# Optimization experiments

Measured on AMD Instinct MI355X. Metric: run time of the kernel, lower is better.

## Reference

```python
import jax, jax.numpy as jnp
import numpy as np

B, D, F, S, R = 2048, 1024, 1024, 64, 16


def _lora_dense(x, ids, kernel, bias, la, lb):
    # base: frozen dense path (stop_gradient mirrors the original module)
    base = x @ jax.lax.stop_gradient(kernel)
    if bias is not None:
        base = base + jax.lax.stop_gradient(bias)
    a = la[ids]            # (B, D, R) per-example adapter gather
    b = lb[ids]            # (B, R, F)
    low = jnp.einsum('bd,bdr->br', x, a)
    delta = jnp.einsum('br,brf->bf', low, b)
    return base + delta


def setup_inputs() -> dict:
    key = jax.random.key(0)
    ks = jax.random.split(key, 32)
    i = iter(range(32))
    d = {}
    d['carry'] = jax.random.normal(ks[next(i)], (B, F), jnp.float32)
    d['inputs'] = jax.random.normal(ks[next(i)], (B, D), jnp.float32)
    d['adapter_ids'] = jax.random.randint(ks[next(i)], (B,), 0, S)
    kscale = 1.0 / np.sqrt(D)
    for g in ['ir', 'iu', 'ic']:
        d[f'w_{g}'] = jax.random.normal(ks[next(i)], (D, F), jnp.float32) * kscale
        d[f'bias_{g}'] = jax.random.normal(ks[next(i)], (F,), jnp.float32) * 0.01
        d[f'la_{g}'] = jax.random.normal(ks[next(i)], (S, D, R), jnp.float32) * 0.02
        d[f'lb_{g}'] = jax.random.normal(ks[next(i)], (S, R, F), jnp.float32) * 0.01
    for g in ['rr', 'ru', 'rc']:
        d[f'w_{g}'] = jax.random.normal(ks[next(i)], (F, F), jnp.float32) * kscale
        d[f'la_{g}'] = jax.random.normal(ks[next(i)], (S, F, R), jnp.float32) * 0.02
        d[f'lb_{g}'] = jax.random.normal(ks[next(i)], (S, R, F), jnp.float32) * 0.01
    return d


def reference(carry, inputs, adapter_ids,
              w_ir, bias_ir, la_ir, lb_ir,
              w_iu, bias_iu, la_iu, lb_iu,
              w_ic, bias_ic, la_ic, lb_ic,
              w_rr, la_rr, lb_rr,
              w_ru, la_ru, lb_ru,
              w_rc, la_rc, lb_rc):
    ids = adapter_ids
    reset = jax.nn.sigmoid(
        _lora_dense(inputs, ids, w_ir, bias_ir, la_ir, lb_ir)
        + _lora_dense(carry, ids, w_rr, None, la_rr, lb_rr))
    update = jax.nn.sigmoid(
        _lora_dense(inputs, ids, w_iu, bias_iu, la_iu, lb_iu)
        + _lora_dense(carry, ids, w_ru, None, la_ru, lb_ru))
    candidate = jnp.tanh(
        _lora_dense(inputs, ids, w_ic, bias_ic, la_ic, lb_ic)
        + reset * _lora_dense(carry, ids, w_rc, None, la_rc, lb_rc))
    new_carry = (1.0 - update) * candidate + update * carry
    return new_carry
```

## Files before the change

kernel.cpp:

```cpp
#include <hip/hip_runtime.h>
#include <stdint.h>

#define B_  2048
#define D_  1024
#define F_  1024
#define S_  64
#define R_  16

typedef __attribute__((ext_vector_type(8))) short  s16x8;
typedef __attribute__((ext_vector_type(4))) unsigned short u16x4;
typedef __attribute__((ext_vector_type(8))) unsigned short u16x8;
typedef __attribute__((ext_vector_type(4))) float  f32x4;

__device__ __forceinline__ unsigned short f2b(float f){
  unsigned u = __float_as_uint(f);
  u = u + 0x7fffu + ((u >> 16) & 1u);
  return (unsigned short)(u >> 16);
}
__device__ __forceinline__ float b2f(unsigned short s){
  return __uint_as_float(((unsigned)s) << 16);
}

__device__ __forceinline__ void gload16(const void* g, void* l){
  __builtin_amdgcn_global_load_lds((const __attribute__((address_space(1))) unsigned int*)g,
                                   (__attribute__((address_space(3))) unsigned int*)l, 16, 0, 0);
}

#define W0OFF 0
#define W1OFF 2097152
#define W2OFF 4194304
#define W3OFF 5242880

__global__ __launch_bounds__(256) void prep_kernel(
    const float* __restrict__ x, const float* __restrict__ carry,
    unsigned short* __restrict__ XC,
    const float* __restrict__ w_ir, const float* __restrict__ w_rr,
    const float* __restrict__ w_iu, const float* __restrict__ w_ru,
    const float* __restrict__ w_ic, const float* __restrict__ w_rc,
    unsigned short* __restrict__ Wt_all,
    const int* __restrict__ ids, int* __restrict__ starts, int* __restrict__ order){
  int bx = blockIdx.x;
  int t = threadIdx.x;
  if (bx < 2048){
    int i = bx * 256 + t;
    int b = i >> 8;
    int j = (i & 255) * 4;
    float4 xv = *(const float4*)&x[(size_t)b*D_ + j];
    float4 cv = *(const float4*)&carry[(size_t)b*F_ + j];
    u16x4 xs, cs;
    xs[0]=f2b(xv.x); xs[1]=f2b(xv.y); xs[2]=f2b(xv.z); xs[3]=f2b(xv.w);
    cs[0]=f2b(cv.x); cs[1]=f2b(cv.y); cs[2]=f2b(cv.z); cs[3]=f2b(cv.w);
    *(u16x4*)&XC[(size_t)b*2048 + j]        = xs;
    *(u16x4*)&XC[(size_t)b*2048 + 1024 + j] = cs;
    return;
  }
  if (bx < 3584){
    int wb = bx - 2048;
    int g = wb >> 8, xb = wb & 255;
    const float* W; unsigned short* O; int st, ko;
    switch(g){
      case 0:  W=w_ir; O=Wt_all+W0OFF; st=2048; ko=0;    break;
      case 1:  W=w_rr; O=Wt_all+W0OFF; st=2048; ko=1024; break;
      case 2:  W=w_iu; O=Wt_all+W1OFF; st=2048; ko=0;    break;
      case 3:  W=w_ru; O=Wt_all+W1OFF; st=2048; ko=1024; break;
      case 4:  W=w_ic; O=Wt_all+W2OFF; st=1024; ko=0;    break;
      default: W=w_rc; O=Wt_all+W3OFF; st=1024; ko=0;    break;
    }
    __shared__ unsigned short T[64][72];
    int n0 = (xb & 15) * 64;
    int k0 = (xb >> 4) * 64;
    int c4 = (t & 15) * 4;
    int kk = t >> 4;
    #pragma unroll
    for (int i = 0; i < 4; i++){
      int k = kk + i*16;
      float4 v = *(const float4*)&W[(size_t)(k0+k)*F_ + n0 + c4];
      T[c4+0][k] = f2b(v.x); T[c4+1][k] = f2b(v.y); T[c4+2][k] = f2b(v.z); T[c4+3][k] = f2b(v.w);
    }
    __syncthreads();
    int n = t >> 2, ch = (t & 3) * 16;
    u16x8 a = *(const u16x8*)&T[n][ch];
    u16x8 b = *(const u16x8*)&T[n][ch+8];
    *(u16x8*)&O[(size_t)(n0+n)*st + ko + k0 + ch]     = a;
    *(u16x8*)&O[(size_t)(n0+n)*st + ko + k0 + ch + 8] = b;
    return;
  }
  __shared__ int cnt[S_]; __shared__ int off[S_+1]; __shared__ int cur[S_];
  if (t < S_) cnt[t] = 0;
  __syncthreads();
  for (int b = t; b < B_; b += 256) atomicAdd(&cnt[ids[b]], 1);
  __syncthreads();
  if (t == 0){ off[0] = 0; for (int s2 = 0; s2 < S_; s2++) off[s2+1] = off[s2] + cnt[s2]; }
  __syncthreads();
  if (t < S_) cur[t] = off[t];
  __syncthreads();
  for (int b = t; b < B_; b += 256){ int p = atomicAdd(&cur[ids[b]], 1); order[p] = b; }
  if (t < S_+1) starts[t] = off[t];
}

__global__ __launch_bounds__(256, 4) void gemm_low_kernel(
    const unsigned short* __restrict__ XC,
    const unsigned short* __restrict__ Wt_all,
    unsigned short* __restrict__ Yall,
    const float* __restrict__ la_ir, const float* __restrict__ la_iu,
    const float* __restrict__ la_ic, const float* __restrict__ la_rr,
    const float* __restrict__ la_ru, const float* __restrict__ la_rc,
    const int* __restrict__ starts, const int* __restrict__ order,
    float* __restrict__ low){
  __shared__ __align__(16) unsigned short smem[16512];
  int t = threadIdx.x;
  int bx = blockIdx.x;

  if (bx >= 512){
    int lb = bx - 512;
    int s = lb & 63, g = lb >> 6;
    const float* la;
    switch(g){ case 0: la=la_ir; break; case 1: la=la_iu; break; case 2: la=la_ic; break;
               case 3: la=la_rr; break; case 4: la=la_ru; break; default: la=la_rc; break; }
    int kofs = (g < 3) ? 0 : 1024;
    la += (size_t)s * D_ * R_;
    unsigned short* LA = smem;
    for (int i4 = t; i4 < D_*R_/4; i4 += 256){
      float4 v = *(const float4*)&la[i4*4];
      int d = i4 >> 2, r0 = (i4 & 3) * 4;
      LA[(r0+0)*1032 + d] = f2b(v.x);
      LA[(r0+1)*1032 + d] = f2b(v.y);
      LA[(r0+2)*1032 + d] = f2b(v.z);
      LA[(r0+3)*1032 + d] = f2b(v.w);
    }
    __syncthreads();
    int start = starts[s], cnt = starts[s+1] - start;
    if (cnt == 0) return;
    int lane = t & 63, wave = t >> 6;
    int l15 = lane & 15, kq = (lane >> 4) * 8;
    int ntiles = (cnt + 15) >> 4;
    for (int mt = wave*2; mt < ntiles; mt += 8){
      bool two = (mt + 1 < ntiles);
      int m0 = mt*16 + l15;       if (m0 >= cnt) m0 = cnt - 1;
      int m1 = (mt+1)*16 + l15;   if (m1 >= cnt) m1 = cnt - 1;
      int e0 = order[start + m0];
      int e1 = two ? order[start + m1] : e0;
      const unsigned short* A0 = XC + (size_t)e0*2048 + kofs + kq;
      const unsigned short* A1 = XC + (size_t)e1*2048 + kofs + kq;
      const unsigned short* Bp = &LA[l15*1032 + kq];
      f32x4 acc0 = {}, acc1 = {};
      #pragma unroll 4
      for (int kt = 0; kt < 1024; kt += 32){
        s16x8 a0 = *(const s16x8*)(A0 + kt);
        s16x8 a1 = *(const s16x8*)(A1 + kt);
        s16x8 b  = *(const s16x8*)(Bp + kt);
        acc0 = __builtin_amdgcn_mfma_f32_16x16x32_bf16(a0, b, acc0, 0, 0, 0);
        acc1 = __builtin_amdgcn_mfma_f32_16x16x32_bf16(a1, b, acc1, 0, 0, 0);
      }
      int rowb = (lane >> 4) * 4;
      #pragma unroll
      for (int i = 0; i < 4; i++){
        int m = mt*16 + rowb + i;
        if (m < cnt){
          int e = order[start + m];
          low[((size_t)g*B_ + e)*R_ + l15] = acc0[i];
        }
      }
      if (two){
        #pragma unroll
        for (int i = 0; i < 4; i++){
          int m = (mt+1)*16 + rowb + i;
          if (m < cnt){
            int e = order[start + m];
            low[((size_t)g*B_ + e)*R_ + l15] = acc1[i];
          }
        }
      }
    }
    return;
  }

  int u = bx >> 7;
  int tile = bx & 127;
  int K = (u < 2) ? 2048 : 1024;
  int kofs = (u == 3) ? 1024 : 0;
  const size_t uoffs[4] = {W0OFF, W1OFF, W2OFF, W3OFF};
  const unsigned short* Wt = Wt_all + uoffs[u];
  unsigned short* Y = Yall + (size_t)u * ((size_t)B_ * F_);

  unsigned short (*As)[4096] = (unsigned short(*)[4096])smem;
  unsigned short (*Bs)[4096] = (unsigned short(*)[4096])(smem + 8192);

  int lane = t & 63, wave = t >> 6;
  int mt = tile >> 3, nt = tile & 7;
  int row0 = mt * 128, col0 = nt * 128;
  int wrow = (wave >> 1) * 64, wcol = (wave & 1) * 64;

  int arow = t >> 2;
  int achk = ((t & 3) ^ ((t >> 3) & 3)) * 8;

  const unsigned short* Ab  = XC + (size_t)(row0 + arow) * 2048 + kofs + achk;
  const unsigned short* Ab2 = Ab + (size_t)64 * 2048;
  const unsigned short* Bb  = Wt + (size_t)(col0 + arow) * K + achk;
  const unsigned short* Bb2 = Bb + (size_t)64 * K;

  int l15 = lane & 15;
  int kof = (((lane >> 4) ^ ((l15 >> 1) & 3)) * 8);
  f32x4 acc[4][4] = {};

  gload16(Ab,  &As[0][t*8]);  gload16(Ab2, &As[0][2048 + t*8]);
  gload16(Bb,  &Bs[0][t*8]);  gload16(Bb2, &Bs[0][2048 + t*8]);
  __syncthreads();

  int cur = 0;
  for (int kt = 32; kt < K; kt += 32){
    int nxt = cur ^ 1;
    gload16(Ab  + kt, &As[nxt][t*8]);  gload16(Ab2 + kt, &As[nxt][2048 + t*8]);
    gload16(Bb  + kt, &Bs[nxt][t*8]);  gload16(Bb2 + kt, &Bs[nxt][2048 + t*8]);
    s16x8 af[4], bfr[4];
    #pragma unroll
    for (int m = 0; m < 4; m++)
      af[m] = *(const s16x8*)&As[cur][(wrow + m*16 + l15)*32 + kof];
    #pragma unroll
    for (int n = 0; n < 4; n++)
      bfr[n] = *(const s16x8*)&Bs[cur][(wcol + n*16 + l15)*32 + kof];
    __builtin_amdgcn_s_setprio(1);
    #pragma unroll
    for (int m = 0; m < 4; m++){
      #pragma unroll
      for (int n = 0; n < 4; n++){
        acc[m][n] = __builtin_amdgcn_mfma_f32_16x16x32_bf16(af[m], bfr[n], acc[m][n], 0, 0, 0);
      }
    }
    __builtin_amdgcn_s_setprio(0);
    __syncthreads();
    cur = nxt;
  }
  {
    s16x8 af[4], bfr[4];
    #pragma unroll
    for (int m = 0; m < 4; m++)
      af[m] = *(const s16x8*)&As[cur][(wrow + m*16 + l15)*32 + kof];
    #pragma unroll
    for (int n = 0; n < 4; n++)
      bfr[n] = *(const s16x8*)&Bs[cur][(wcol + n*16 + l15)*32 + kof];
    #pragma unroll
    for (int m = 0; m < 4; m++){
      #pragma unroll
      for (int n = 0; n < 4; n++){
        acc[m][n] = __builtin_amdgcn_mfma_f32_16x16x32_bf16(af[m], bfr[n], acc[m][n], 0, 0, 0);
      }
    }
  }

  int orow = row0 + wrow + (lane >> 4) * 4;
  int ocol = col0 + wcol + l15;
  #pragma unroll
  for (int m = 0; m < 4; m++){
    #pragma unroll
    for (int n = 0; n < 4; n++){
      #pragma unroll
      for (int i = 0; i < 4; i++){
        Y[(size_t)(orow + m*16 + i) * F_ + ocol + n*16] = f2b(acc[m][n][i]);
      }
    }
  }
}

__global__ __launch_bounds__(256) void delta_final_kernel(
    const float* __restrict__ carry,
    const float* __restrict__ bias_ir, const float* __restrict__ bias_iu,
    const float* __restrict__ bias_ic,
    const float* __restrict__ lb_ir, const float* __restrict__ lb_rr,
    const float* __restrict__ lb_iu, const float* __restrict__ lb_ru,
    const float* __restrict__ lb_ic, const float* __restrict__ lb_rc,
    const int* __restrict__ starts, const int* __restrict__ order,
    const float* __restrict__ low, const unsigned short* __restrict__ Yall,
    float* __restrict__ out){
  int s = blockIdx.x;
  int c0 = blockIdx.y * 128;
  __shared__ unsigned short Bsm[3 * 128 * 40];
  int t = threadIdx.x;
  const float* lbp[6] = {lb_ir, lb_rr, lb_iu, lb_ru, lb_ic, lb_rc};
  #pragma unroll
  for (int j = 0; j < 6; j++){
    const float* lb = lbp[j] + (size_t)s * R_ * F_;
    unsigned short* Bj = &Bsm[(j >> 1)*5120 + (j & 1)*16];
    #pragma unroll
    for (int it = 0; it < 2; it++){
      int idx = t + it*256;
      int r = idx >> 5, c4 = (idx & 31) * 4;
      float4 v = *(const float4*)&lb[(size_t)r*F_ + c0 + c4];
      Bj[(c4+0)*40 + r] = f2b(v.x);
      Bj[(c4+1)*40 + r] = f2b(v.y);
      Bj[(c4+2)*40 + r] = f2b(v.z);
      Bj[(c4+3)*40 + r] = f2b(v.w);
    }
  }
  __syncthreads();
  int start = starts[s], cnt = starts[s+1] - start;
  if (cnt == 0) return;
  int lane = t & 63, wave = t >> 6;
  int l15 = lane & 15, kq = (lane >> 4) * 8;
  int ntiles = (cnt + 15) >> 4;
  const unsigned short* Y0 = Yall + 0*(size_t)B_*F_;
  const unsigned short* Y1 = Yall + 1*(size_t)B_*F_;
  const unsigned short* Y2 = Yall + 2*(size_t)B_*F_;
  const unsigned short* Y3 = Yall + 3*(size_t)B_*F_;
  int k8 = kq & 15; bool hi = (kq >= 16);
  for (int pt = wave; pt < ntiles*2; pt += 4){
    int mt = pt >> 1, cf0 = (pt & 1) * 4;
    int m = mt*16 + l15; if (m >= cnt) m = cnt - 1;
    int e = order[start + m];
    s16x8 a_r, a_u, a_c1 = {}, a_c2 = {};
    {
      const float* p = &low[((size_t)(hi ? 3 : 0)*B_ + e)*R_ + k8];
      float4 v0 = *(const float4*)p, v1 = *(const float4*)(p+4);
      a_r[0]=f2b(v0.x); a_r[1]=f2b(v0.y); a_r[2]=f2b(v0.z); a_r[3]=f2b(v0.w);
      a_r[4]=f2b(v1.x); a_r[5]=f2b(v1.y); a_r[6]=f2b(v1.z); a_r[7]=f2b(v1.w);
    }
    {
      const float* p = &low[((size_t)(hi ? 4 : 1)*B_ + e)*R_ + k8];
      float4 v0 = *(const float4*)p, v1 = *(const float4*)(p+4);
      a_u[0]=f2b(v0.x); a_u[1]=f2b(v0.y); a_u[2]=f2b(v0.z); a_u[3]=f2b(v0.w);
      a_u[4]=f2b(v1.x); a_u[5]=f2b(v1.y); a_u[6]=f2b(v1.z); a_u[7]=f2b(v1.w);
    }
    if (!hi){
      const float* p = &low[((size_t)2*B_ + e)*R_ + k8];
      float4 v0 = *(const float4*)p, v1 = *(const float4*)(p+4);
      a_c1[0]=f2b(v0.x); a_c1[1]=f2b(v0.y); a_c1[2]=f2b(v0.z); a_c1[3]=f2b(v0.w);
      a_c1[4]=f2b(v1.x); a_c1[5]=f2b(v1.y); a_c1[6]=f2b(v1.z); a_c1[7]=f2b(v1.w);
    } else {
      const float* p = &low[((size_t)5*B_ + e)*R_ + k8];
      float4 v0 = *(const float4*)p, v1 = *(const float4*)(p+4);
      a_c2[0]=f2b(v0.x); a_c2[1]=f2b(v0.y); a_c2[2]=f2b(v0.z); a_c2[3]=f2b(v0.w);
      a_c2[4]=f2b(v1.x); a_c2[5]=f2b(v1.y); a_c2[6]=f2b(v1.z); a_c2[7]=f2b(v1.w);
    }
    int rowb = (lane >> 4) * 4;
    int erow[4]; bool wok[4];
    #pragma unroll
    for (int i = 0; i < 4; i++){
      int mm = mt*16 + rowb + i;
      wok[i] = (mm < cnt);
      erow[i] = order[start + (wok[i] ? mm : cnt - 1)];
    }
    #pragma unroll
    for (int cf = cf0; cf < cf0 + 4; cf++){
      int col = cf*16 + l15;
      s16x8 b_r = *(const s16x8*)&Bsm[0*5120 + col*40 + kq];
      s16x8 b_u = *(const s16x8*)&Bsm[1*5120 + col*40 + kq];
      s16x8 b_c = *(const s16x8*)&Bsm[2*5120 + col*40 + kq];
      f32x4 zero = {};
      f32x4 dr  = __builtin_amdgcn_mfma_f32_16x16x32_bf16(a_r,  b_r, zero, 0, 0, 0);
      f32x4 du  = __builtin_amdgcn_mfma_f32_16x16x32_bf16(a_u,  b_u, zero, 0, 0, 0);
      f32x4 dic = __builtin_amdgcn_mfma_f32_16x16x32_bf16(a_c1, b_c, zero, 0, 0, 0);
      f32x4 drc = __builtin_amdgcn_mfma_f32_16x16x32_bf16(a_c2, b_c, zero, 0, 0, 0);
      int oc = c0 + col;
      float br = bias_ir[oc], bu = bias_iu[oc], bc = bias_ic[oc];
      #pragma unroll
      for (int i = 0; i < 4; i++){
        if (wok[i]){
          size_t idx = (size_t)erow[i]*F_ + oc;
          float zr  = b2f(Y0[idx]) + br + dr[i];
          float zu  = b2f(Y1[idx]) + bu + du[i];
          float zic = b2f(Y2[idx]) + bc + dic[i];
          float zrc = b2f(Y3[idx]) + drc[i];
          float cv  = carry[idx];
          float rr = 1.f/(1.f+__expf(-zr));
          float uu = 1.f/(1.f+__expf(-zu));
          float a = zic + rr*zrc;
          float ee = __expf(-2.f*fabsf(a));
          float cand = copysignf((1.f-ee)/(1.f+ee), a);
          out[idx] = (1.f-uu)*cand + uu*cv;
        }
      }
    }
  }
}

extern "C" void kernel_launch(void* const* d_in, const int* in_sizes, int n_in,
                              void* d_out, int out_size, void* d_ws, size_t ws_size,
                              hipStream_t stream){
  const float* carry   = (const float*)d_in[0];
  const float* x       = (const float*)d_in[1];
  const int*   ids     = (const int*)d_in[2];
  const float* w_ir    = (const float*)d_in[3];
  const float* bias_ir = (const float*)d_in[4];
  const float* la_ir   = (const float*)d_in[5];
  const float* lb_ir   = (const float*)d_in[6];
  const float* w_iu    = (const float*)d_in[7];
  const float* bias_iu = (const float*)d_in[8];
  const float* la_iu   = (const float*)d_in[9];
  const float* lb_iu   = (const float*)d_in[10];
  const float* w_ic    = (const float*)d_in[11];
  const float* bias_ic = (const float*)d_in[12];
  const float* la_ic   = (const float*)d_in[13];
  const float* lb_ic   = (const float*)d_in[14];
  const float* w_rr    = (const float*)d_in[15];
  const float* la_rr   = (const float*)d_in[16];
  const float* lb_rr   = (const float*)d_in[17];
  const float* w_ru    = (const float*)d_in[18];
  const float* la_ru   = (const float*)d_in[19];
  const float* lb_ru   = (const float*)d_in[20];
  const float* w_rc    = (const float*)d_in[21];
  const float* la_rc   = (const float*)d_in[22];
  const float* lb_rc   = (const float*)d_in[23];

  char* ws = (char*)d_ws;
  unsigned short* XC     = (unsigned short*)(ws + 0);
  unsigned short* Wt_all = (unsigned short*)(ws + 8388608);
  unsigned short* Yall   = (unsigned short*)(ws + 20971520);
  float* low  = (float*)(ws + 37748736);
  int* starts = (int*)(ws + 38535168);
  int* order  = (int*)(ws + 38536192);

  prep_kernel<<<dim3(3585), dim3(256), 0, stream>>>(x, carry, XC,
                                                    w_ir, w_rr, w_iu, w_ru, w_ic, w_rc,
                                                    Wt_all, ids, starts, order);
  gemm_low_kernel<<<dim3(896), dim3(256), 0, stream>>>(XC, Wt_all, Yall,
                                                       la_ir, la_iu, la_ic,
                                                       la_rr, la_ru, la_rc,
                                                       starts, order, low);
  delta_final_kernel<<<dim3(64, 8), dim3(256), 0, stream>>>(carry, bias_ir, bias_iu, bias_ic,
                                                            lb_ir, lb_rr, lb_iu, lb_ru,
                                                            lb_ic, lb_rc,
                                                            starts, order, low, Yall,
                                                            (float*)d_out);
}
```

Before: 83.28 us.

## Split fused K=2048 GEMMs into six uniform K=1024 GEMMs and store low in bf16

Each weight is now transposed into its own 1024x1024 block instead of being concatenated along K, and the main GEMM runs six uniform K=1024 problems (768 tiles) rather than four with mixed K. This balances work across blocks and puts the low-rank blocks first in the grid. The input-plus-recurrent sums are added in the epilogue, which reads two extra bf16 Y planes. The low-rank projection uses one tile per wave with two split-K accumulators and stores bf16 instead of fp32, so the final kernel skips its conversions. In exchange, Y traffic grows by half and the extra bf16 rounding of partial sums may cost some accuracy.

```diff
diff --git a/kernel.cpp b/kernel.cpp
--- a/kernel.cpp
+++ b/kernel.cpp
@@ -26,10 +26,6 @@
                                    (__attribute__((address_space(3))) unsigned int*)l, 16, 0, 0);
 }
 
-#define W0OFF 0
-#define W1OFF 2097152
-#define W2OFF 4194304
-#define W3OFF 5242880
 
 __global__ __launch_bounds__(256) void prep_kernel(
     const float* __restrict__ x, const float* __restrict__ carry,
@@ -57,15 +53,10 @@
   if (bx < 3584){
     int wb = bx - 2048;
     int g = wb >> 8, xb = wb & 255;
-    const float* W; unsigned short* O; int st, ko;
-    switch(g){
-      case 0:  W=w_ir; O=Wt_all+W0OFF; st=2048; ko=0;    break;
-      case 1:  W=w_rr; O=Wt_all+W0OFF; st=2048; ko=1024; break;
-      case 2:  W=w_iu; O=Wt_all+W1OFF; st=2048; ko=0;    break;
-      case 3:  W=w_ru; O=Wt_all+W1OFF; st=2048; ko=1024; break;
-      case 4:  W=w_ic; O=Wt_all+W2OFF; st=1024; ko=0;    break;
-      default: W=w_rc; O=Wt_all+W3OFF; st=1024; ko=0;    break;
-    }
+    const float* W;
+    switch(g){ case 0: W=w_ir; break; case 1: W=w_rr; break; case 2: W=w_iu; break;
+               case 3: W=w_ru; break; case 4: W=w_ic; break; default: W=w_rc; break; }
+    unsigned short* O = Wt_all + (size_t)g * 1048576;
     __shared__ unsigned short T[64][72];
     int n0 = (xb & 15) * 64;
     int k0 = (xb >> 4) * 64;
@@ -81,8 +72,8 @@
     int n = t >> 2, ch = (t & 3) * 16;
     u16x8 a = *(const u16x8*)&T[n][ch];
     u16x8 b = *(const u16x8*)&T[n][ch+8];
-    *(u16x8*)&O[(size_t)(n0+n)*st + ko + k0 + ch]     = a;
-    *(u16x8*)&O[(size_t)(n0+n)*st + ko + k0 + ch + 8] = b;
+    *(u16x8*)&O[(size_t)(n0+n)*1024 + k0 + ch]     = a;
+    *(u16x8*)&O[(size_t)(n0+n)*1024 + k0 + ch + 8] = b;
     return;
   }
   __shared__ int cnt[S_]; __shared__ int off[S_+1]; __shared__ int cur[S_];
@@ -106,14 +97,13 @@
     const float* __restrict__ la_ic, const float* __restrict__ la_rr,
     const float* __restrict__ la_ru, const float* __restrict__ la_rc,
     const int* __restrict__ starts, const int* __restrict__ order,
-    float* __restrict__ low){
+    unsigned short* __restrict__ lowb){
   __shared__ __align__(16) unsigned short smem[16512];
   int t = threadIdx.x;
   int bx = blockIdx.x;
 
-  if (bx >= 512){
-    int lb = bx - 512;
-    int s = lb & 63, g = lb >> 6;
+  if (bx < 384){
+    int s = bx & 63, g = bx >> 6;
     const float* la;
     switch(g){ case 0: la=la_ir; break; case 1: la=la_iu; break; case 2: la=la_ic; break;
                case 3: la=la_rr; break; case 4: la=la_ru; break; default: la=la_rc; break; }
@@ -134,53 +124,40 @@
     int lane = t & 63, wave = t >> 6;
     int l15 = lane & 15, kq = (lane >> 4) * 8;
     int ntiles = (cnt + 15) >> 4;
-    for (int mt = wave*2; mt < ntiles; mt += 8){
-      bool two = (mt + 1 < ntiles);
-      int m0 = mt*16 + l15;       if (m0 >= cnt) m0 = cnt - 1;
-      int m1 = (mt+1)*16 + l15;   if (m1 >= cnt) m1 = cnt - 1;
+    for (int mt = wave; mt < ntiles; mt += 4){
+      int m0 = mt*16 + l15; if (m0 >= cnt) m0 = cnt - 1;
       int e0 = order[start + m0];
-      int e1 = two ? order[start + m1] : e0;
       const unsigned short* A0 = XC + (size_t)e0*2048 + kofs + kq;
-      const unsigned short* A1 = XC + (size_t)e1*2048 + kofs + kq;
       const unsigned short* Bp = &LA[l15*1032 + kq];
-      f32x4 acc0 = {}, acc1 = {};
+      f32x4 accA = {}, accB = {};
       #pragma unroll 4
-      for (int kt = 0; kt < 1024; kt += 32){
+      for (int kt = 0; kt < 512; kt += 32){
         s16x8 a0 = *(const s16x8*)(A0 + kt);
-        s16x8 a1 = *(const s16x8*)(A1 + kt);
-        s16x8 b  = *(const s16x8*)(Bp + kt);
-        acc0 = __builtin_amdgcn_mfma_f32_16x16x32_bf16(a0, b, acc0, 0, 0, 0);
-        acc1 = __builtin_amdgcn_mfma_f32_16x16x32_bf16(a1, b, acc1, 0, 0, 0);
-      }
+        s16x8 b0 = *(const s16x8*)(Bp + kt);
+        s16x8 a1 = *(const s16x8*)(A0 + 512 + kt);
+        s16x8 b1 = *(const s16x8*)(Bp + 512 + kt);
+        accA = __builtin_amdgcn_mfma_f32_16x16x32_bf16(a0, b0, accA, 0, 0, 0);
+        accB = __builtin_amdgcn_mfma_f32_16x16x32_bf16(a1, b1, accB, 0, 0, 0);
+      }
+      f32x4 acc = accA + accB;
       int rowb = (lane >> 4) * 4;
       #pragma unroll
       for (int i = 0; i < 4; i++){
         int m = mt*16 + rowb + i;
         if (m < cnt){
           int e = order[start + m];
-          low[((size_t)g*B_ + e)*R_ + l15] = acc0[i];
+          lowb[((size_t)g*B_ + e)*R_ + l15] = f2b(acc[i]);
         }
       }
-      if (two){
-        #pragma unroll
-        for (int i = 0; i < 4; i++){
-          int m = (mt+1)*16 + rowb + i;
-          if (m < cnt){
-            int e = order[start + m];
-            low[((size_t)g*B_ + e)*R_ + l15] = acc1[i];
-          }
-        }
-      }
     }
     return;
   }
 
-  int u = bx >> 7;
-  int tile = bx & 127;
-  int K = (u < 2) ? 2048 : 1024;
-  int kofs = (u == 3) ? 1024 : 0;
-  const size_t uoffs[4] = {W0OFF, W1OFF, W2OFF, W3OFF};
-  const unsigned short* Wt = Wt_all + uoffs[u];
+  int bid = bx - 384;
+  int u = bid >> 7;
+  int tile = bid & 127;
+  int kofs = (u & 1) << 10;
+  const unsigned short* Wt = Wt_all + (size_t)u * 1048576;
   unsigned short* Y = Yall + (size_t)u * ((size_t)B_ * F_);
 
   unsigned short (*As)[4096] = (unsigned short(*)[4096])smem;
@@ -196,8 +173,8 @@
 
   const unsigned short* Ab  = XC + (size_t)(row0 + arow) * 2048 + kofs + achk;
   const unsigned short* Ab2 = Ab + (size_t)64 * 2048;
-  const unsigned short* Bb  = Wt + (size_t)(col0 + arow) * K + achk;
-  const unsigned short* Bb2 = Bb + (size_t)64 * K;
+  const unsigned short* Bb  = Wt + (size_t)(col0 + arow) * 1024 + achk;
+  const unsigned short* Bb2 = Bb + (size_t)64 * 1024;
 
   int l15 = lane & 15;
   int kof = (((lane >> 4) ^ ((l15 >> 1) & 3)) * 8);
@@ -208,7 +185,7 @@
   __syncthreads();
 
   int cur = 0;
-  for (int kt = 32; kt < K; kt += 32){
+  for (int kt = 32; kt < 1024; kt += 32){
     int nxt = cur ^ 1;
     gload16(Ab  + kt, &As[nxt][t*8]);  gload16(Ab2 + kt, &As[nxt][2048 + t*8]);
     gload16(Bb  + kt, &Bs[nxt][t*8]);  gload16(Bb2 + kt, &Bs[nxt][2048 + t*8]);
@@ -270,7 +247,7 @@
     const float* __restrict__ lb_iu, const float* __restrict__ lb_ru,
     const float* __restrict__ lb_ic, const float* __restrict__ lb_rc,
     const int* __restrict__ starts, const int* __restrict__ order,
-    const float* __restrict__ low, const unsigned short* __restrict__ Yall,
+    const unsigned short* __restrict__ lowb, const unsigned short* __restrict__ Yall,
     float* __restrict__ out){
   int s = blockIdx.x;
   int c0 = blockIdx.y * 128;
@@ -302,35 +279,18 @@
   const unsigned short* Y1 = Yall + 1*(size_t)B_*F_;
   const unsigned short* Y2 = Yall + 2*(size_t)B_*F_;
   const unsigned short* Y3 = Yall + 3*(size_t)B_*F_;
+  const unsigned short* Y4 = Yall + 4*(size_t)B_*F_;
+  const unsigned short* Y5 = Yall + 5*(size_t)B_*F_;
   int k8 = kq & 15; bool hi = (kq >= 16);
   for (int pt = wave; pt < ntiles*2; pt += 4){
     int mt = pt >> 1, cf0 = (pt & 1) * 4;
     int m = mt*16 + l15; if (m >= cnt) m = cnt - 1;
     int e = order[start + m];
     s16x8 a_r, a_u, a_c1 = {}, a_c2 = {};
-    {
-      const float* p = &low[((size_t)(hi ? 3 : 0)*B_ + e)*R_ + k8];
-      float4 v0 = *(const float4*)p, v1 = *(const float4*)(p+4);
-      a_r[0]=f2b(v0.x); a_r[1]=f2b(v0.y); a_r[2]=f2b(v0.z); a_r[3]=f2b(v0.w);
-      a_r[4]=f2b(v1.x); a_r[5]=f2b(v1.y); a_r[6]=f2b(v1.z); a_r[7]=f2b(v1.w);
-    }
-    {
-      const float* p = &low[((size_t)(hi ? 4 : 1)*B_ + e)*R_ + k8];
-      float4 v0 = *(const float4*)p, v1 = *(const float4*)(p+4);
-      a_u[0]=f2b(v0.x); a_u[1]=f2b(v0.y); a_u[2]=f2b(v0.z); a_u[3]=f2b(v0.w);
-      a_u[4]=f2b(v1.x); a_u[5]=f2b(v1.y); a_u[6]=f2b(v1.z); a_u[7]=f2b(v1.w);
-    }
-    if (!hi){
-      const float* p = &low[((size_t)2*B_ + e)*R_ + k8];
-      float4 v0 = *(const float4*)p, v1 = *(const float4*)(p+4);
-      a_c1[0]=f2b(v0.x); a_c1[1]=f2b(v0.y); a_c1[2]=f2b(v0.z); a_c1[3]=f2b(v0.w);
-      a_c1[4]=f2b(v1.x); a_c1[5]=f2b(v1.y); a_c1[6]=f2b(v1.z); a_c1[7]=f2b(v1.w);
-    } else {
-      const float* p = &low[((size_t)5*B_ + e)*R_ + k8];
-      float4 v0 = *(const float4*)p, v1 = *(const float4*)(p+4);
-      a_c2[0]=f2b(v0.x); a_c2[1]=f2b(v0.y); a_c2[2]=f2b(v0.z); a_c2[3]=f2b(v0.w);
-      a_c2[4]=f2b(v1.x); a_c2[5]=f2b(v1.y); a_c2[6]=f2b(v1.z); a_c2[7]=f2b(v1.w);
-    }
+    a_r = *(const s16x8*)&lowb[((size_t)(hi ? 3 : 0)*B_ + e)*R_ + k8];
+    a_u = *(const s16x8*)&lowb[((size_t)(hi ? 4 : 1)*B_ + e)*R_ + k8];
+    if (!hi) a_c1 = *(const s16x8*)&lowb[((size_t)2*B_ + e)*R_ + k8];
+    else     a_c2 = *(const s16x8*)&lowb[((size_t)5*B_ + e)*R_ + k8];
     int rowb = (lane >> 4) * 4;
     int erow[4]; bool wok[4];
     #pragma unroll
@@ -356,10 +316,10 @@
       for (int i = 0; i < 4; i++){
         if (wok[i]){
           size_t idx = (size_t)erow[i]*F_ + oc;
-          float zr  = b2f(Y0[idx]) + br + dr[i];
-          float zu  = b2f(Y1[idx]) + bu + du[i];
-          float zic = b2f(Y2[idx]) + bc + dic[i];
-          float zrc = b2f(Y3[idx]) + drc[i];
+          float zr  = b2f(Y0[idx]) + b2f(Y1[idx]) + br + dr[i];
+          float zu  = b2f(Y2[idx]) + b2f(Y3[idx]) + bu + du[i];
+          float zic = b2f(Y4[idx]) + bc + dic[i];
+          float zrc = b2f(Y5[idx]) + drc[i];
           float cv  = carry[idx];
           float rr = 1.f/(1.f+__expf(-zr));
           float uu = 1.f/(1.f+__expf(-zu));
@@ -405,20 +365,20 @@
   unsigned short* XC     = (unsigned short*)(ws + 0);
   unsigned short* Wt_all = (unsigned short*)(ws + 8388608);
   unsigned short* Yall   = (unsigned short*)(ws + 20971520);
-  float* low  = (float*)(ws + 37748736);
-  int* starts = (int*)(ws + 38535168);
-  int* order  = (int*)(ws + 38536192);
+  unsigned short* lowb   = (unsigned short*)(ws + 46137344);
+  int* starts = (int*)(ws + 46530560);
+  int* order  = (int*)(ws + 46531584);
 
   prep_kernel<<<dim3(3585), dim3(256), 0, stream>>>(x, carry, XC,
                                                     w_ir, w_rr, w_iu, w_ru, w_ic, w_rc,
                                                     Wt_all, ids, starts, order);
-  gemm_low_kernel<<<dim3(896), dim3(256), 0, stream>>>(XC, Wt_all, Yall,
-                                                       la_ir, la_iu, la_ic,
-                                                       la_rr, la_ru, la_rc,
-                                                       starts, order, low);
+  gemm_low_kernel<<<dim3(1152), dim3(256), 0, stream>>>(XC, Wt_all, Yall,
+                                                        la_ir, la_iu, la_ic,
+                                                        la_rr, la_ru, la_rc,
+                                                        starts, order, lowb);
   delta_final_kernel<<<dim3(64, 8), dim3(256), 0, stream>>>(carry, bias_ir, bias_iu, bias_ic,
                                                             lb_ir, lb_rr, lb_iu, lb_ru,
                                                             lb_ic, lb_rc,
-                                                            starts, order, low, Yall,
+                                                            starts, order, lowb, Yall,
                                                             (float*)d_out);
 }
```

Measured after the change: 89.85 us. 1.08x slower.
